# Kernel tuning notes

Measured on AMD Instinct MI355X. Metric: run time of the kernel, lower is better.

The kernel has to match this reference:

```python
import jax, jax.numpy as jnp
import numpy as np

D_MODEL = 2048
N_HEADS = 16
HEAD_DIM = D_MODEL // N_HEADS
B, L = 2, 2048
ROPE_BASE = 10000.0
NEG_INF = -1e30


def _rope_cache(seq_len, head_dim):
    inv_freq = 1.0 / (ROPE_BASE ** (np.arange(0, head_dim, 2, dtype=np.float32) / head_dim))
    t = np.arange(seq_len, dtype=np.float32)
    freqs = np.outer(t, inv_freq)                      # (L, hd/2)
    emb = np.concatenate([freqs, freqs], axis=-1)      # (L, hd)
    return jnp.asarray(np.cos(emb)), jnp.asarray(np.sin(emb))


def setup_inputs() -> dict:
    key = jax.random.key(0)
    kx, kq, ko, kl = jax.random.split(key, 4)
    x = jax.random.normal(kx, (B, L, D_MODEL), dtype=jnp.float32)
    w_qkv = jax.random.normal(kq, (3 * D_MODEL, D_MODEL), dtype=jnp.float32) / np.sqrt(D_MODEL)
    w_out = jax.random.normal(ko, (D_MODEL, D_MODEL), dtype=jnp.float32) / np.sqrt(D_MODEL)
    # key-padding style keep-mask: keep first `lengths[b]` tokens (pos 0 always kept)
    lengths = jax.random.randint(kl, (B,), L // 2, L + 1)
    attn_keep_mask = jnp.arange(L)[None, :] < lengths[:, None]
    cos, sin = _rope_cache(L, HEAD_DIM)
    return {"x": x, "attn_keep_mask": attn_keep_mask, "cos": cos, "sin": sin,
            "w_qkv": w_qkv, "w_out": w_out}


def _rotate_half(t):
    h = t.shape[-1] // 2
    return jnp.concatenate([-t[..., h:], t[..., :h]], axis=-1)


def _apply_rope(t, cos, sin):
    # t: (B, H, L, hd); cos/sin: (L, hd)
    return t * cos[None, None] + _rotate_half(t) * sin[None, None]


def reference(x, attn_keep_mask, cos, sin, w_qkv, w_out):
    Bv, Lv, Dv = x.shape
    qkv = jnp.einsum('bld,ed->ble', x, w_qkv)                      # (B, L, 3D)
    q, k, v = jnp.split(qkv, 3, axis=-1)
    def heads(t):
        return t.reshape(Bv, Lv, N_HEADS, HEAD_DIM).transpose(0, 2, 1, 3)  # (B,H,L,hd)
    q, k, v = heads(q), heads(k), heads(v)
    q = _apply_rope(q, cos, sin)
    k = _apply_rope(k, cos, sin)
    scale = 1.0 / np.sqrt(HEAD_DIM)
    scores = jnp.einsum('bhqd,bhkd->bhqk', q, k) * scale            # (B,H,L,L)
    causal = jnp.tril(jnp.ones((Lv, Lv), dtype=bool))               # (L,L)
    allowed = causal[None, None] & attn_keep_mask[:, None, None, :]  # keep keys
    scores = jnp.where(allowed, scores, NEG_INF)
    probs = jax.nn.softmax(scores, axis=-1)
    attn = jnp.einsum('bhqk,bhkd->bhqd', probs, v)                  # (B,H,L,hd)
    out = attn.transpose(0, 2, 1, 3).reshape(Bv, Lv, Dv)
    out = jnp.where(attn_keep_mask[:, :, None], out, 0.0)
    return jnp.einsum('bld,ed->ble', out, w_out)
```

## Files before the change

### kernel.cpp

```cpp
#include <hip/hip_runtime.h>

typedef unsigned short u16;
typedef u16 u16x8 __attribute__((ext_vector_type(8)));
typedef u16 u16x4 __attribute__((ext_vector_type(4)));
typedef __bf16 bf16x8_t __attribute__((ext_vector_type(8)));
typedef float f32x4 __attribute__((ext_vector_type(4)));

#define GLOBAL_AS __attribute__((address_space(1)))
#define LDS_AS __attribute__((address_space(3)))

__device__ __forceinline__ float bf2f(u16 v) {
    return __uint_as_float(((unsigned int)v) << 16);
}
__device__ __forceinline__ u16 f2bf(float f) {
    unsigned int u = __float_as_uint(f);
    u += 0x7fff + ((u >> 16) & 1);
    return (u16)(u >> 16);
}

__device__ __forceinline__ f32x4 mfma_bf16(u16x8 a, u16x8 b, f32x4 c) {
    return __builtin_amdgcn_mfma_f32_16x16x32_bf16(
        __builtin_bit_cast(bf16x8_t, a), __builtin_bit_cast(bf16x8_t, b), c, 0, 0, 0);
}

__device__ __forceinline__ float red16_max(float x) {
    int t;
    t = __builtin_amdgcn_update_dpp(0, __builtin_bit_cast(int, x), 0xB1, 0xF, 0xF, true);
    x = fmaxf(x, __builtin_bit_cast(float, t));
    t = __builtin_amdgcn_update_dpp(0, __builtin_bit_cast(int, x), 0x4E, 0xF, 0xF, true);
    x = fmaxf(x, __builtin_bit_cast(float, t));
    t = __builtin_amdgcn_update_dpp(0, __builtin_bit_cast(int, x), 0x124, 0xF, 0xF, true);
    x = fmaxf(x, __builtin_bit_cast(float, t));
    t = __builtin_amdgcn_update_dpp(0, __builtin_bit_cast(int, x), 0x128, 0xF, 0xF, true);
    x = fmaxf(x, __builtin_bit_cast(float, t));
    return x;
}
__device__ __forceinline__ float red16_sum(float x) {
    int t;
    t = __builtin_amdgcn_update_dpp(0, __builtin_bit_cast(int, x), 0xB1, 0xF, 0xF, true);
    x += __builtin_bit_cast(float, t);
    t = __builtin_amdgcn_update_dpp(0, __builtin_bit_cast(int, x), 0x4E, 0xF, 0xF, true);
    x += __builtin_bit_cast(float, t);
    t = __builtin_amdgcn_update_dpp(0, __builtin_bit_cast(int, x), 0x124, 0xF, 0xF, true);
    x += __builtin_bit_cast(float, t);
    t = __builtin_amdgcn_update_dpp(0, __builtin_bit_cast(int, x), 0x128, 0xF, 0xF, true);
    x += __builtin_bit_cast(float, t);
    return x;
}

__global__ __launch_bounds__(256) void cvt_kernel(const float* __restrict__ in,
                                                  u16* __restrict__ out, int n4) {
    int i = blockIdx.x * 256 + threadIdx.x;
    if (i >= n4) return;
    float4 f = ((const float4*)in)[i];
    u16x4 o = { f2bf(f.x), f2bf(f.y), f2bf(f.z), f2bf(f.w) };
    ((u16x4*)out)[i] = o;
}

__global__ __launch_bounds__(256) void mask_prep(const unsigned char* __restrict__ raw,
                                                 int* __restrict__ lens) {
    const int b = blockIdx.x;
    const int tid = threadIdx.x, lane = tid & 63, wid = tid >> 6;
    const unsigned char b0 = raw[0];
    int cnt = 0;
    for (int i = tid; i < 2048; i += 256) {
        const size_t idx = (size_t)b * 2048 + i;
        bool v;
        if (b0 == 0) {
            v = ((const float*)raw)[idx] != 0.0f;
        } else if (b0 == 0x80) {
            v = ((const u16*)raw)[idx] != 0;
        } else {
            const int stride = raw[1] ? 1 : (raw[2] ? 2 : (raw[4] ? 4 : 8));
            v = raw[idx * stride] != 0;
        }
        cnt += v ? 1 : 0;
    }
    cnt += __shfl_xor(cnt, 1);
    cnt += __shfl_xor(cnt, 2);
    cnt += __shfl_xor(cnt, 4);
    cnt += __shfl_xor(cnt, 8);
    cnt += __shfl_xor(cnt, 16);
    cnt += __shfl_xor(cnt, 32);
    __shared__ int wsum[4];
    if (lane == 0) wsum[wid] = cnt;
    __syncthreads();
    if (tid == 0) lens[b] = wsum[0] + wsum[1] + wsum[2] + wsum[3];
}

template <int MODE>
__global__ __launch_bounds__(512, 2) void gemm_bt(
    const u16* __restrict__ A, const u16* __restrict__ B,
    int M, int N, int K, int nbx,
    u16* __restrict__ qp, u16* __restrict__ kp, u16* __restrict__ vp,
    float* __restrict__ outf) {
    __shared__ u16 lds[3 * 24576];
    const int tid  = threadIdx.x;
    const int lane = tid & 63;
    const int wid  = tid >> 6;
    const int wm   = wid >> 1;
    const int wn   = wid & 1;

    const int cpx = (int)gridDim.x >> 3;
    const int bid = blockIdx.x;
    const int swz = (bid & 7) * cpx + (bid >> 3);
    const int bx = swz % nbx, by = swz / nbx;
    const int brow = by * 256;
    const int bcol = bx * 128;

    f32x4 acc[4][4];
#pragma unroll
    for (int m = 0; m < 4; ++m)
#pragma unroll
        for (int n = 0; n < 4; ++n)
            acc[m][n] = (f32x4){0.f, 0.f, 0.f, 0.f};

    const int scol  = (((tid & 7) ^ ((tid >> 3) & 7)) << 3);
    const int arow0 = tid >> 3;
    const u16* aBase = A + (size_t)(brow + arow0) * K + scol;
    const u16* bBase = B + (size_t)(bcol + arow0) * K + scol;

    auto stage = [&](int kt, int bb) {
        char* base = (char*)lds + bb * 49152;
        const u16* as = aBase + kt * 64;
        const u16* bs = bBase + kt * 64;
#pragma unroll
        for (int i = 0; i < 4; ++i)
            __builtin_amdgcn_global_load_lds((const GLOBAL_AS void*)(as + (size_t)(i * 64) * K),
                (LDS_AS void*)(base + i * 8192 + wid * 1024), 16, 0, 0);
#pragma unroll
        for (int i = 0; i < 2; ++i)
            __builtin_amdgcn_global_load_lds((const GLOBAL_AS void*)(bs + (size_t)(i * 64) * K),
                (LDS_AS void*)(base + 32768 + i * 8192 + wid * 1024), 16, 0, 0);
    };

    const int nkt = K >> 6;
    stage(0, 0);
    stage(1, 1);

    int bufc = 0;
    for (int kt = 0; kt < nkt; ++kt) {
        if (kt + 1 < nkt) asm volatile("s_waitcnt vmcnt(6)" ::: "memory");
        else              asm volatile("s_waitcnt vmcnt(0)" ::: "memory");
        __builtin_amdgcn_s_barrier();
        __builtin_amdgcn_sched_barrier(0);

        if (kt + 2 < nkt) {
            int nb = bufc + 2; if (nb >= 3) nb -= 3;
            stage(kt + 2, nb);
        }

        const u16* lA = lds + bufc * 24576;
        const u16* lB = lA + 16384;
        u16x8 af[4][2], bfr[4][2];
#pragma unroll
        for (int m = 0; m < 4; ++m)
#pragma unroll
            for (int ks = 0; ks < 2; ++ks) {
                const int row = wm * 64 + m * 16 + (lane & 15);
                const int g = ((ks << 2) + (lane >> 4)) ^ (lane & 7);
                af[m][ks] = *(const u16x8*)&lA[row * 64 + (g << 3)];
            }
#pragma unroll
        for (int n = 0; n < 4; ++n)
#pragma unroll
            for (int ks = 0; ks < 2; ++ks) {
                const int row = wn * 64 + n * 16 + (lane & 15);
                const int g = ((ks << 2) + (lane >> 4)) ^ (lane & 7);
                bfr[n][ks] = *(const u16x8*)&lB[row * 64 + (g << 3)];
            }

        __builtin_amdgcn_s_setprio(1);
#pragma unroll
        for (int ks = 0; ks < 2; ++ks)
#pragma unroll
            for (int m = 0; m < 4; ++m)
#pragma unroll
                for (int n = 0; n < 4; ++n)
                    acc[m][n] = mfma_bf16(af[m][ks], bfr[n][ks], acc[m][n]);
        __builtin_amdgcn_s_setprio(0);

        ++bufc; if (bufc == 3) bufc = 0;
    }

#pragma unroll
    for (int m = 0; m < 4; ++m) {
#pragma unroll
        for (int n = 0; n < 4; ++n) {
#pragma unroll
            for (int j = 0; j < 4; ++j) {
                const int row = brow + wm * 64 + m * 16 + (lane >> 4) * 4 + j;
                const int col = bcol + wn * 64 + n * 16 + (lane & 15);
                const float val = acc[m][n][j];
                if (MODE == 0) {
                    const int part = col >> 11;
                    const int e = col & 2047;
                    const int hh = e >> 7, dd = e & 127;
                    const int bb = row >> 11, ll = row & 2047;
                    u16* dst = (part == 0) ? qp : (part == 1) ? kp : vp;
                    dst[((size_t)(bb * 16 + hh) * 2048 + ll) * 128 + dd] = f2bf(val);
                } else {
                    outf[(size_t)row * N + col] = val;
                }
            }
        }
    }
}

__global__ __launch_bounds__(256) void rope_kernel(u16* __restrict__ qk,
                                                   const float* __restrict__ cosp,
                                                   const float* __restrict__ sinp) {
    const int gid  = blockIdx.x * 4 + (threadIdx.x >> 6);
    const int lane = threadIdx.x & 63;
    const int l    = gid & 2047;
    u16* row = qk + (size_t)gid * 128;
    const int d1 = lane, d2 = lane + 64;
    const float v1 = bf2f(row[d1]);
    const float v2 = bf2f(row[d2]);
    const float c1 = cosp[l * 128 + d1], s1 = sinp[l * 128 + d1];
    const float c2 = cosp[l * 128 + d2], s2 = sinp[l * 128 + d2];
    row[d1] = f2bf(v1 * c1 - v2 * s1);
    row[d2] = f2bf(v2 * c2 + v1 * s2);
}

__global__ __launch_bounds__(256, 2) void attn_kernel(
    const u16* __restrict__ Q, const u16* __restrict__ K, const u16* __restrict__ V,
    const int* __restrict__ lens, u16* __restrict__ O) {
    __shared__ u16 lK[64 * 136];
    __shared__ u16 lVT[128 * 72];
    __shared__ u16 lP[4 * 16 * 72];

    const int tid = threadIdx.x, lane = tid & 63, wid = tid >> 6;
    const int g   = blockIdx.x;
    const int xcd = g & 7;
    const int s   = g >> 3;
    const int jA  = s >> 2;
    const int bh  = (xcd << 2) | (s & 3);
    const int b   = bh >> 4;
    const int h   = bh & 15;
    const u16* qb = Q + (size_t)bh * 2048 * 128;
    const u16* kb = K + (size_t)bh * 2048 * 128;
    const u16* vb = V + (size_t)bh * 2048 * 128;
    const int lenb = lens[b];
    const int str = lane;
    const int sdc = wid;
    const float scale2 = 0.12754245006257017f;
    const float THR = 32.0f;
    u16* lPw = lP + wid * (16 * 72);

    for (int half = 0; half < 2; ++half) {
        const int jq = half ? jA : (31 - jA);
        const int q0w = jq * 64 + wid * 16;

        if (jq * 64 >= lenb) {
#pragma unroll
            for (int j = 0; j < 4; ++j) {
                const int qq = q0w + (lane >> 4) * 4 + j;
#pragma unroll
                for (int n = 0; n < 8; ++n) {
                    const int d = n * 16 + (lane & 15);
                    O[((size_t)b * 2048 + qq) * 2048 + h * 128 + d] = 0;
                }
            }
            continue;
        }

        const int nt_full = jq + 1;
        const int lt = (lenb + 63) >> 6;
        const int ktiles = nt_full < lt ? nt_full : lt;

        u16x8 aq[4];
#pragma unroll
        for (int kc = 0; kc < 4; ++kc)
            aq[kc] = *(const u16x8*)(qb + (size_t)(q0w + (lane & 15)) * 128 + kc * 32 + (lane >> 4) * 8);

        float ms[4], ls[4];
        f32x4 ao[8];
#pragma unroll
        for (int j = 0; j < 4; ++j) { ms[j] = -1e30f; ls[j] = 0.f; }
#pragma unroll
        for (int n = 0; n < 8; ++n) ao[n] = (f32x4){0.f, 0.f, 0.f, 0.f};

        u16x8 pk[4], pv[4];
        {
            const u16* ks = kb + (size_t)str * 128 + sdc * 32;
            const u16* vs = vb + (size_t)str * 128 + sdc * 32;
#pragma unroll
            for (int i = 0; i < 4; ++i) { pk[i] = *(const u16x8*)(ks + i * 8); pv[i] = *(const u16x8*)(vs + i * 8); }
        }
        __syncthreads();
#pragma unroll
        for (int i = 0; i < 4; ++i) {
            *(u16x8*)&lK[str * 136 + sdc * 32 + i * 8] = pk[i];
#pragma unroll
            for (int e = 0; e < 8; ++e)
                lVT[(sdc * 32 + i * 8 + e) * 72 + str] = pv[i][e];
        }
        __syncthreads();

        for (int t = 0; t < ktiles; ++t) {
            const bool pf = (t + 1 < ktiles);
            if (pf) {
                const u16* ks = kb + (size_t)((t + 1) * 64 + str) * 128 + sdc * 32;
                const u16* vs = vb + (size_t)((t + 1) * 64 + str) * 128 + sdc * 32;
#pragma unroll
                for (int i = 0; i < 4; ++i) { pk[i] = *(const u16x8*)(ks + i * 8); pv[i] = *(const u16x8*)(vs + i * 8); }
            }
            const int kv0 = t * 64;

            f32x4 sv4[4];
#pragma unroll
            for (int n = 0; n < 4; ++n) sv4[n] = (f32x4){0.f, 0.f, 0.f, 0.f};
#pragma unroll
            for (int kc = 0; kc < 4; ++kc) {
                u16x8 bk[4];
#pragma unroll
                for (int n = 0; n < 4; ++n)
                    bk[n] = *(const u16x8*)&lK[(n * 16 + (lane & 15)) * 136 + kc * 32 + (lane >> 4) * 8];
#pragma unroll
                for (int n = 0; n < 4; ++n)
                    sv4[n] = mfma_bf16(aq[kc], bk[n], sv4[n]);
            }

            const bool needmask = (t == jq) || (kv0 + 64 > lenb);
#pragma unroll
            for (int j = 0; j < 4; ++j) {
                const int row = (lane >> 4) * 4 + j;
                float sv[4];
                if (needmask) {
                    const int qq = q0w + row;
                    const int bound = (qq < lenb - 1) ? qq : (lenb - 1);
#pragma unroll
                    for (int n = 0; n < 4; ++n) {
                        const int kk = kv0 + n * 16 + (lane & 15);
                        sv[n] = (kk <= bound) ? sv4[n][j] : -1e30f;
                    }
                } else {
#pragma unroll
                    for (int n = 0; n < 4; ++n) sv[n] = sv4[n][j];
                }
                const float rm = red16_max(fmaxf(fmaxf(sv[0], sv[1]), fmaxf(sv[2], sv[3])));
                const float mo = ms[j];
                const bool grow = !__all(rm <= mo + THR);
                if (grow) {
                    const float mn = fmaxf(mo, rm);
                    ms[j] = mn;
                    const float alpha = exp2f((mo - mn) * scale2);
                    ls[j] *= alpha;
#pragma unroll
                    for (int n = 0; n < 8; ++n) ao[n][j] *= alpha;
                }
                const float mk = ms[j] * scale2;
                float rs = 0.f;
#pragma unroll
                for (int n = 0; n < 4; ++n) {
                    const float p = exp2f(fmaf(sv[n], scale2, -mk));
                    rs += p;
                    lPw[row * 72 + n * 16 + (lane & 15)] = f2bf(p);
                }
                ls[j] += red16_sum(rs);
            }

#pragma unroll
            for (int kc = 0; kc < 2; ++kc) {
                u16x8 ap = *(const u16x8*)&lPw[(lane & 15) * 72 + kc * 32 + (lane >> 4) * 8];
#pragma unroll
                for (int n = 0; n < 8; ++n) {
                    u16x8 bv = *(const u16x8*)&lVT[(n * 16 + (lane & 15)) * 72 + kc * 32 + (lane >> 4) * 8];
                    ao[n] = mfma_bf16(ap, bv, ao[n]);
                }
            }

            if (pf) {
                __syncthreads();
#pragma unroll
                for (int i = 0; i < 4; ++i) {
                    *(u16x8*)&lK[str * 136 + sdc * 32 + i * 8] = pk[i];
#pragma unroll
                    for (int e = 0; e < 8; ++e)
                        lVT[(sdc * 32 + i * 8 + e) * 72 + str] = pv[i][e];
                }
                __syncthreads();
            }
        }

#pragma unroll
        for (int j = 0; j < 4; ++j) {
            const int qq = q0w + (lane >> 4) * 4 + j;
            const float inv = (qq < lenb) ? (1.f / ls[j]) : 0.f;
#pragma unroll
            for (int n = 0; n < 8; ++n) {
                const int d = n * 16 + (lane & 15);
                O[((size_t)b * 2048 + qq) * 2048 + h * 128 + d] = f2bf(ao[n][j] * inv);
            }
        }
    }
}

extern "C" void kernel_launch(void* const* d_in, const int* in_sizes, int n_in,
                              void* d_out, int out_size, void* d_ws, size_t ws_size,
                              hipStream_t stream) {
    const float* x      = (const float*)d_in[0];
    const unsigned char* maskraw = (const unsigned char*)d_in[1];
    const float* cosp   = (const float*)d_in[2];
    const float* sinp   = (const float*)d_in[3];
    const float* w_qkv  = (const float*)d_in[4];
    const float* w_out  = (const float*)d_in[5];
    float* out = (float*)d_out;

    char* ws = (char*)d_ws;
    size_t off = 0;
    auto alloc = [&](size_t bytes) {
        char* p = ws + off;
        off += (bytes + 255) & ~(size_t)255;
        return p;
    };
    u16* xb    = (u16*)alloc((size_t)4096 * 2048 * 2);
    u16* wqkvb = (u16*)alloc((size_t)6144 * 2048 * 2);
    u16* woutb = (u16*)alloc((size_t)2048 * 2048 * 2);
    u16* qB    = (u16*)alloc((size_t)65536 * 128 * 2);
    u16* kB    = (u16*)alloc((size_t)65536 * 128 * 2);
    u16* vB    = (u16*)alloc((size_t)65536 * 128 * 2);
    u16* attno = (u16*)alloc((size_t)4096 * 2048 * 2);
    int* lens  = (int*)alloc(256);

    cvt_kernel<<<dim3(4096 * 2048 / 4 / 256), dim3(256), 0, stream>>>(x, xb, 4096 * 2048 / 4);
    cvt_kernel<<<dim3(6144 * 2048 / 4 / 256), dim3(256), 0, stream>>>(w_qkv, wqkvb, 6144 * 2048 / 4);
    cvt_kernel<<<dim3(2048 * 2048 / 4 / 256), dim3(256), 0, stream>>>(w_out, woutb, 2048 * 2048 / 4);
    mask_prep<<<dim3(2), dim3(256), 0, stream>>>(maskraw, lens);

    gemm_bt<0><<<dim3(768), dim3(512), 0, stream>>>(xb, wqkvb, 4096, 6144, 2048, 48,
                                                    qB, kB, vB, nullptr);
    rope_kernel<<<dim3(131072 / 4), dim3(256), 0, stream>>>(qB, cosp, sinp);
    attn_kernel<<<dim3(512), dim3(256), 0, stream>>>(qB, kB, vB, lens, attno);
    gemm_bt<1><<<dim3(256), dim3(512), 0, stream>>>(attno, woutb, 4096, 2048, 2048, 16,
                                                    nullptr, nullptr, nullptr, out);
}
```

Baseline: 297.6 us.

## Split attention into one block per query tile with XOR-swizzled LDS layouts

Each attention block previously handled a paired heavy and light query tile. Now each block handles one query tile, and the grid doubles to 1024 blocks, launched heaviest tiles first. The padded LDS strides are replaced by XOR-swizzled unpadded layouts for K, V-transpose and P to avoid bank conflicts while shrinking shared memory, and launch bounds rise to allow 4 blocks per CU for higher occupancy. The risk is that register pressure under the tighter bound may cause spills, and the balance now depends on the hardware scheduler rather than explicit pairing.

```diff
diff --git a/kernel.cpp b/kernel.cpp
--- a/kernel.cpp
+++ b/kernel.cpp
@@ -223,176 +223,179 @@
     row[d2] = f2bf(v2 * c2 + v1 * s2);
 }
 
-__global__ __launch_bounds__(256, 2) void attn_kernel(
+__global__ __launch_bounds__(256, 4) void attn_kernel(
     const u16* __restrict__ Q, const u16* __restrict__ K, const u16* __restrict__ V,
     const int* __restrict__ lens, u16* __restrict__ O) {
-    __shared__ u16 lK[64 * 136];
-    __shared__ u16 lVT[128 * 72];
-    __shared__ u16 lP[4 * 16 * 72];
+    __shared__ u16 lK[64 * 128];
+    __shared__ u16 lVT[128 * 64];
+    __shared__ u16 lP[4 * 16 * 64];
 
     const int tid = threadIdx.x, lane = tid & 63, wid = tid >> 6;
     const int g   = blockIdx.x;
     const int xcd = g & 7;
-    const int s   = g >> 3;
-    const int jA  = s >> 2;
-    const int bh  = (xcd << 2) | (s & 3);
+    const int r   = g >> 3;
+    const int jq  = 31 - (r >> 2);
+    const int bh  = (xcd << 2) | (r & 3);
     const int b   = bh >> 4;
     const int h   = bh & 15;
     const u16* qb = Q + (size_t)bh * 2048 * 128;
     const u16* kb = K + (size_t)bh * 2048 * 128;
     const u16* vb = V + (size_t)bh * 2048 * 128;
     const int lenb = lens[b];
+    const int q0w = jq * 64 + wid * 16;
     const int str = lane;
     const int sdc = wid;
     const float scale2 = 0.12754245006257017f;
     const float THR = 32.0f;
-    u16* lPw = lP + wid * (16 * 72);
-
-    for (int half = 0; half < 2; ++half) {
-        const int jq = half ? jA : (31 - jA);
-        const int q0w = jq * 64 + wid * 16;
-
-        if (jq * 64 >= lenb) {
-#pragma unroll
-            for (int j = 0; j < 4; ++j) {
-                const int qq = q0w + (lane >> 4) * 4 + j;
-#pragma unroll
-                for (int n = 0; n < 8; ++n) {
-                    const int d = n * 16 + (lane & 15);
-                    O[((size_t)b * 2048 + qq) * 2048 + h * 128 + d] = 0;
-                }
-            }
-            continue;
-        }
-
-        const int nt_full = jq + 1;
-        const int lt = (lenb + 63) >> 6;
-        const int ktiles = nt_full < lt ? nt_full : lt;
-
-        u16x8 aq[4];
-#pragma unroll
-        for (int kc = 0; kc < 4; ++kc)
-            aq[kc] = *(const u16x8*)(qb + (size_t)(q0w + (lane & 15)) * 128 + kc * 32 + (lane >> 4) * 8);
-
-        float ms[4], ls[4];
-        f32x4 ao[8];
-#pragma unroll
-        for (int j = 0; j < 4; ++j) { ms[j] = -1e30f; ls[j] = 0.f; }
-#pragma unroll
-        for (int n = 0; n < 8; ++n) ao[n] = (f32x4){0.f, 0.f, 0.f, 0.f};
-
-        u16x8 pk[4], pv[4];
-        {
-            const u16* ks = kb + (size_t)str * 128 + sdc * 32;
-            const u16* vs = vb + (size_t)str * 128 + sdc * 32;
-#pragma unroll
-            for (int i = 0; i < 4; ++i) { pk[i] = *(const u16x8*)(ks + i * 8); pv[i] = *(const u16x8*)(vs + i * 8); }
-        }
-        __syncthreads();
-#pragma unroll
-        for (int i = 0; i < 4; ++i) {
-            *(u16x8*)&lK[str * 136 + sdc * 32 + i * 8] = pk[i];
-#pragma unroll
-            for (int e = 0; e < 8; ++e)
-                lVT[(sdc * 32 + i * 8 + e) * 72 + str] = pv[i][e];
-        }
-        __syncthreads();
-
-        for (int t = 0; t < ktiles; ++t) {
-            const bool pf = (t + 1 < ktiles);
-            if (pf) {
-                const u16* ks = kb + (size_t)((t + 1) * 64 + str) * 128 + sdc * 32;
-                const u16* vs = vb + (size_t)((t + 1) * 64 + str) * 128 + sdc * 32;
-#pragma unroll
-                for (int i = 0; i < 4; ++i) { pk[i] = *(const u16x8*)(ks + i * 8); pv[i] = *(const u16x8*)(vs + i * 8); }
-            }
-            const int kv0 = t * 64;
-
-            f32x4 sv4[4];
-#pragma unroll
-            for (int n = 0; n < 4; ++n) sv4[n] = (f32x4){0.f, 0.f, 0.f, 0.f};
-#pragma unroll
-            for (int kc = 0; kc < 4; ++kc) {
-                u16x8 bk[4];
-#pragma unroll
-                for (int n = 0; n < 4; ++n)
-                    bk[n] = *(const u16x8*)&lK[(n * 16 + (lane & 15)) * 136 + kc * 32 + (lane >> 4) * 8];
-#pragma unroll
-                for (int n = 0; n < 4; ++n)
-                    sv4[n] = mfma_bf16(aq[kc], bk[n], sv4[n]);
-            }
-
-            const bool needmask = (t == jq) || (kv0 + 64 > lenb);
-#pragma unroll
-            for (int j = 0; j < 4; ++j) {
-                const int row = (lane >> 4) * 4 + j;
-                float sv[4];
-                if (needmask) {
-                    const int qq = q0w + row;
-                    const int bound = (qq < lenb - 1) ? qq : (lenb - 1);
-#pragma unroll
-                    for (int n = 0; n < 4; ++n) {
-                        const int kk = kv0 + n * 16 + (lane & 15);
-                        sv[n] = (kk <= bound) ? sv4[n][j] : -1e30f;
-                    }
-                } else {
-#pragma unroll
-                    for (int n = 0; n < 4; ++n) sv[n] = sv4[n][j];
-                }
-                const float rm = red16_max(fmaxf(fmaxf(sv[0], sv[1]), fmaxf(sv[2], sv[3])));
-                const float mo = ms[j];
-                const bool grow = !__all(rm <= mo + THR);
-                if (grow) {
-                    const float mn = fmaxf(mo, rm);
-                    ms[j] = mn;
-                    const float alpha = exp2f((mo - mn) * scale2);
-                    ls[j] *= alpha;
-#pragma unroll
-                    for (int n = 0; n < 8; ++n) ao[n][j] *= alpha;
-                }
-                const float mk = ms[j] * scale2;
-                float rs = 0.f;
-#pragma unroll
-                for (int n = 0; n < 4; ++n) {
-                    const float p = exp2f(fmaf(sv[n], scale2, -mk));
-                    rs += p;
-                    lPw[row * 72 + n * 16 + (lane & 15)] = f2bf(p);
-                }
-                ls[j] += red16_sum(rs);
-            }
-
-#pragma unroll
-            for (int kc = 0; kc < 2; ++kc) {
-                u16x8 ap = *(const u16x8*)&lPw[(lane & 15) * 72 + kc * 32 + (lane >> 4) * 8];
-#pragma unroll
-                for (int n = 0; n < 8; ++n) {
-                    u16x8 bv = *(const u16x8*)&lVT[(n * 16 + (lane & 15)) * 72 + kc * 32 + (lane >> 4) * 8];
-                    ao[n] = mfma_bf16(ap, bv, ao[n]);
-                }
-            }
-
-            if (pf) {
-                __syncthreads();
-#pragma unroll
-                for (int i = 0; i < 4; ++i) {
-                    *(u16x8*)&lK[str * 136 + sdc * 32 + i * 8] = pk[i];
-#pragma unroll
-                    for (int e = 0; e < 8; ++e)
-                        lVT[(sdc * 32 + i * 8 + e) * 72 + str] = pv[i][e];
-                }
-                __syncthreads();
-            }
-        }
-
+    u16* lPw = lP + wid * 1024;
+
+    if (jq * 64 >= lenb) {
 #pragma unroll
         for (int j = 0; j < 4; ++j) {
             const int qq = q0w + (lane >> 4) * 4 + j;
-            const float inv = (qq < lenb) ? (1.f / ls[j]) : 0.f;
 #pragma unroll
             for (int n = 0; n < 8; ++n) {
                 const int d = n * 16 + (lane & 15);
-                O[((size_t)b * 2048 + qq) * 2048 + h * 128 + d] = f2bf(ao[n][j] * inv);
-            }
+                O[((size_t)b * 2048 + qq) * 2048 + h * 128 + d] = 0;
+            }
+        }
+        return;
+    }
+
+    const int nt_full = jq + 1;
+    const int lt = (lenb + 63) >> 6;
+    const int ktiles = nt_full < lt ? nt_full : lt;
+
+    u16x8 aq[4];
+#pragma unroll
+    for (int kc = 0; kc < 4; ++kc)
+        aq[kc] = *(const u16x8*)(qb + (size_t)(q0w + (lane & 15)) * 128 + kc * 32 + (lane >> 4) * 8);
+
+    float ms[4], ls[4];
+    f32x4 ao[8];
+#pragma unroll
+    for (int j = 0; j < 4; ++j) { ms[j] = -1e30f; ls[j] = 0.f; }
+#pragma unroll
+    for (int n = 0; n < 8; ++n) ao[n] = (f32x4){0.f, 0.f, 0.f, 0.f};
+
+    u16x8 pk[4], pv[4];
+    {
+        const u16* ks = kb + (size_t)str * 128 + sdc * 32;
+        const u16* vs = vb + (size_t)str * 128 + sdc * 32;
+#pragma unroll
+        for (int i = 0; i < 4; ++i) { pk[i] = *(const u16x8*)(ks + i * 8); pv[i] = *(const u16x8*)(vs + i * 8); }
+    }
+#pragma unroll
+    for (int i = 0; i < 4; ++i) {
+        *(u16x8*)&lK[str * 128 + (((sdc * 4 + i) ^ (str & 7)) << 3)] = pk[i];
+#pragma unroll
+        for (int e = 0; e < 8; ++e) {
+            const int d = sdc * 32 + i * 8 + e;
+            lVT[d * 64 + (((str >> 3) ^ (d & 7)) << 3) + (str & 7)] = pv[i][e];
+        }
+    }
+    __syncthreads();
+
+    for (int t = 0; t < ktiles; ++t) {
+        const bool pf = (t + 1 < ktiles);
+        if (pf) {
+            const u16* ks = kb + (size_t)((t + 1) * 64 + str) * 128 + sdc * 32;
+            const u16* vs = vb + (size_t)((t + 1) * 64 + str) * 128 + sdc * 32;
+#pragma unroll
+            for (int i = 0; i < 4; ++i) { pk[i] = *(const u16x8*)(ks + i * 8); pv[i] = *(const u16x8*)(vs + i * 8); }
+        }
+        const int kv0 = t * 64;
+
+        f32x4 sv4[4];
+#pragma unroll
+        for (int n = 0; n < 4; ++n) sv4[n] = (f32x4){0.f, 0.f, 0.f, 0.f};
+#pragma unroll
+        for (int kc = 0; kc < 4; ++kc) {
+            u16x8 bk[4];
+#pragma unroll
+            for (int n = 0; n < 4; ++n) {
+                const int rk = n * 16 + (lane & 15);
+                bk[n] = *(const u16x8*)&lK[rk * 128 + (((kc * 4 + (lane >> 4)) ^ (rk & 7)) << 3)];
+            }
+#pragma unroll
+            for (int n = 0; n < 4; ++n)
+                sv4[n] = mfma_bf16(aq[kc], bk[n], sv4[n]);
+        }
+
+        const bool needmask = (t == jq) || (kv0 + 64 > lenb);
+#pragma unroll
+        for (int j = 0; j < 4; ++j) {
+            const int row = (lane >> 4) * 4 + j;
+            float sv[4];
+            if (needmask) {
+                const int qq = q0w + row;
+                const int bound = (qq < lenb - 1) ? qq : (lenb - 1);
+#pragma unroll
+                for (int n = 0; n < 4; ++n) {
+                    const int kk = kv0 + n * 16 + (lane & 15);
+                    sv[n] = (kk <= bound) ? sv4[n][j] : -1e30f;
+                }
+            } else {
+#pragma unroll
+                for (int n = 0; n < 4; ++n) sv[n] = sv4[n][j];
+            }
+            const float rm = red16_max(fmaxf(fmaxf(sv[0], sv[1]), fmaxf(sv[2], sv[3])));
+            const float mo = ms[j];
+            const bool grow = !__all(rm <= mo + THR);
+            if (grow) {
+                const float mn = fmaxf(mo, rm);
+                ms[j] = mn;
+                const float alpha = exp2f((mo - mn) * scale2);
+                ls[j] *= alpha;
+#pragma unroll
+                for (int n = 0; n < 8; ++n) ao[n][j] *= alpha;
+            }
+            const float mk = ms[j] * scale2;
+            float rs = 0.f;
+#pragma unroll
+            for (int n = 0; n < 4; ++n) {
+                const float p = exp2f(fmaf(sv[n], scale2, -mk));
+                rs += p;
+                lPw[row * 64 + (((n * 2 + ((lane & 15) >> 3)) ^ (row & 7)) << 3) + (lane & 7)] = f2bf(p);
+            }
+            ls[j] += red16_sum(rs);
+        }
+
+#pragma unroll
+        for (int kc = 0; kc < 2; ++kc) {
+            const int rp = lane & 15;
+            u16x8 ap = *(const u16x8*)&lPw[rp * 64 + (((kc * 4 + (lane >> 4)) ^ (rp & 7)) << 3)];
+#pragma unroll
+            for (int n = 0; n < 8; ++n) {
+                const int rd = n * 16 + (lane & 15);
+                u16x8 bv = *(const u16x8*)&lVT[rd * 64 + (((kc * 4 + (lane >> 4)) ^ (rd & 7)) << 3)];
+                ao[n] = mfma_bf16(ap, bv, ao[n]);
+            }
+        }
+
+        if (pf) {
+            __syncthreads();
+#pragma unroll
+            for (int i = 0; i < 4; ++i) {
+                *(u16x8*)&lK[str * 128 + (((sdc * 4 + i) ^ (str & 7)) << 3)] = pk[i];
+#pragma unroll
+                for (int e = 0; e < 8; ++e) {
+                    const int d = sdc * 32 + i * 8 + e;
+                    lVT[d * 64 + (((str >> 3) ^ (d & 7)) << 3) + (str & 7)] = pv[i][e];
+                }
+            }
+            __syncthreads();
+        }
+    }
+
+#pragma unroll
+    for (int j = 0; j < 4; ++j) {
+        const int qq = q0w + (lane >> 4) * 4 + j;
+        const float inv = (qq < lenb) ? (1.f / ls[j]) : 0.f;
+#pragma unroll
+        for (int n = 0; n < 8; ++n) {
+            const int d = n * 16 + (lane & 15);
+            O[((size_t)b * 2048 + qq) * 2048 + h * 128 + d] = f2bf(ao[n][j] * inv);
         }
     }
 }
@@ -432,7 +435,7 @@
     gemm_bt<0><<<dim3(768), dim3(512), 0, stream>>>(xb, wqkvb, 4096, 6144, 2048, 48,
                                                     qB, kB, vB, nullptr);
     rope_kernel<<<dim3(131072 / 4), dim3(256), 0, stream>>>(qB, cosp, sinp);
-    attn_kernel<<<dim3(512), dim3(256), 0, stream>>>(qB, kB, vB, lens, attno);
+    attn_kernel<<<dim3(1024), dim3(256), 0, stream>>>(qB, kB, vB, lens, attno);
     gemm_bt<1><<<dim3(256), dim3(512), 0, stream>>>(attno, woutb, 4096, 2048, 2048, 16,
                                                     nullptr, nullptr, nullptr, out);
 }
```

Measured after the change: 405.0 us. +36.1%, slower.
